# Kernel optimization log

Measured on AMD Instinct MI355X. Metric: run time of the kernel, lower is better.

## Reference

```python
import jax, jax.numpy as jnp
import numpy as np
from jax import lax

FILTER_SIZE = 11
N_ITER = 5


def gaussian_kernel1d(inv_theta, spacing, size):
    # distances = spacing * [-(size//2) .. size//2]; zero out center tap
    d = spacing * jnp.arange(-(size // 2), size // 2 + 1, dtype=jnp.float32)
    k = jnp.exp(-(d * inv_theta) ** 2 / 2)
    return k.at[size // 2].set(0.0)


def conv_along_axis(x, kernel, axis):
    # x: (C, *spatial); 1D conv along `axis`, 'same' padding (kernel symmetric -> corr == conv)
    x = jnp.moveaxis(x, axis, -1)
    shp = x.shape
    x2 = x.reshape(-1, 1, shp[-1])  # (M, 1, L)
    K = kernel.shape[0]
    out = lax.conv_general_dilated(
        x2, kernel[None, None, :].astype(x2.dtype), (1,), [(K // 2, K // 2)],
        dimension_numbers=('NCH', 'OIH', 'NCH'))
    return jnp.moveaxis(out.reshape(shp), -1, axis)


def _gaussian_filter_single(xi, inv_theta, spacing):
    # xi: (C, H, W); separable gaussian with per-sample spacing
    for i in range(2):
        k = gaussian_kernel1d(inv_theta[i], spacing[i], FILTER_SIZE)
        xi = conv_along_axis(xi, k, i + 1)
    return xi


_smooth = jax.vmap(_gaussian_filter_single, in_axes=(0, None, 0))


def reference(x, spatial_spacings, smoothness_weight, inv_smoothness_theta):
    n_classes = x.shape[1]
    comp = -jnp.eye(n_classes, dtype=x.dtype)  # -(label_i == label_j)
    negative_unary = x
    for _ in range(N_ITER):
        p = jax.nn.softmax(x, axis=1)
        s = smoothness_weight * _smooth(p, inv_smoothness_theta, spatial_spacings)
        c = jnp.einsum('bchw,cd->bdhw', s, comp)
        x = negative_unary - c
    return jax.nn.log_softmax(x, axis=1)


def setup_inputs() -> dict:
    key = jax.random.key(0)
    k1, = jax.random.split(key, 1)
    B, C, H, W = 16, 16, 384, 384
    return {
        'x': jax.random.normal(k1, (B, C, H, W), dtype=jnp.float32),
        'spatial_spacings': jnp.ones((B, 2), dtype=jnp.float32),
        'smoothness_weight': jnp.asarray(1.0, dtype=jnp.float32),
        'inv_smoothness_theta': jnp.ones((2,), dtype=jnp.float32),
    }
```

## Files before the change

kernel.cpp:

```cpp
#include <hip/hip_runtime.h>

#define BB 16
#define CC 16
#define HH 384
#define WW 384
#define HWSZ (HH*WW)
#define CHW (CC*HWSZ)
#define NPIX (BB*CHW)

#define FT 768
#define ROWS 12
#define HSEGS (HH/ROWS)
#define SROW 408

typedef unsigned short ushortT;

__device__ __forceinline__ float bf2f(ushortT h) {
    union { unsigned u; float f; } c; c.u = ((unsigned)h) << 16; return c.f;
}
__device__ __forceinline__ ushortT f2bf(float f) {
    union { float f; unsigned u; } c; c.f = f;
    unsigned r = c.u + 0x7FFFu + ((c.u >> 16) & 1u);
    return (ushortT)(r >> 16);
}
__device__ __forceinline__ void unpk2(unsigned u, float& lo, float& hi) {
    union { unsigned u; float f; } a, b;
    a.u = u << 16; b.u = u & 0xFFFF0000u;
    lo = a.f; hi = b.f;
}
__device__ __forceinline__ unsigned pk2(float lo, float hi) {
    return ((unsigned)f2bf(hi) << 16) | (unsigned)f2bf(lo);
}
__device__ __forceinline__ void unpk8(const uint4& q, float* v) {
    unpk2(q.x, v[0], v[1]); unpk2(q.y, v[2], v[3]);
    unpk2(q.z, v[4], v[5]); unpk2(q.w, v[6], v[7]);
}
__device__ __forceinline__ uint4 pk8(const float* v) {
    uint4 q;
    q.x = pk2(v[0], v[1]); q.y = pk2(v[2], v[3]);
    q.z = pk2(v[4], v[5]); q.w = pk2(v[6], v[7]);
    return q;
}

template<int MODE>
__global__ __launch_bounds__(FT) void k_fused(
    const void* __restrict__ in0, const ushortT* __restrict__ x0b,
    void* __restrict__ outp, ushortT* __restrict__ x0b_out,
    const float* __restrict__ spacings, const float* __restrict__ invtheta,
    const float* __restrict__ swp)
{
    __shared__ ushortT xp[2][CC][SROW];
    __shared__ __align__(16) float l_lds[WW];

    const int t  = threadIdx.x;
    const int b  = blockIdx.y;
    const int h0 = blockIdx.x * ROWS;

    if (t < 2 * CC * 12) {
        const int buf = t / (CC * 12);
        const int rem = t - buf * (CC * 12);
        const int c = rem / 12, s = rem - (rem / 12) * 12;
        const int e = (s < 4) ? (2 * s) : (392 + 2 * (s - 4));
        *(unsigned*)&xp[buf][c][e] = 0u;
    }

    const float sw  = swp[0];
    const float sch = spacings[b * 2 + 0] * invtheta[0];
    const float scw = spacings[b * 2 + 1] * invtheta[1];
    float kh[5], kw[5];
#pragma unroll
    for (int j = 0; j < 5; ++j) {
        float dh = sch * (float)(j - 5); kh[j] = __expf(-0.5f * dh * dh);
        float dw = scw * (float)(j - 5); kw[j] = __expf(-0.5f * dw * dw);
    }

    const int ca = t / 48, ga = t - (t / 48) * 48;
    const int colB = t >> 1, halfB = (t & 1) * 8;

    const size_t cbase = (size_t)b * CHW + (size_t)ca * HWSZ + (size_t)ga * 8;

    const uint4 z4 = make_uint4(0u, 0u, 0u, 0u);
    uint4 win[11];
    if (MODE >= 1) {
        const ushortT* tin = (const ushortT*)in0;
#pragma unroll
        for (int j = 0; j < 11; ++j) {
            const int r = h0 + j - 5;
            win[j] = ((unsigned)r < HH) ? *(const uint4*)(tin + cbase + (size_t)r * WW) : z4;
        }
    }

    __syncthreads();

    auto row_body = [&](const int h, const int buf) {
        if (MODE == 0) {
            const float* xf = (const float*)in0;
            const float4 A  = *(const float4*)(xf + cbase + (size_t)h * WW);
            const float4 Bq = *(const float4*)(xf + cbase + (size_t)h * WW + 4);
            float v[8] = {A.x, A.y, A.z, A.w, Bq.x, Bq.y, Bq.z, Bq.w};
            const uint4 q = pk8(v);
            *(uint4*)(x0b_out + cbase + (size_t)h * WW) = q;
            *(uint4*)&xp[buf][ca][8 + ga * 8] = q;
        } else {
            const ushortT* tin = (const ushortT*)in0;
            const int nr = h + 6;
            const uint4 nt = (nr < HH) ? *(const uint4*)(tin + cbase + (size_t)nr * WW) : z4;
            const uint4 uq = *(const uint4*)(x0b + cbase + (size_t)h * WW);
            float acc[8];
#pragma unroll
            for (int k = 0; k < 8; ++k) acc[k] = 0.f;
#pragma unroll
            for (int j = 0; j < 5; ++j) {
                float e1[8], e2[8];
                unpk8(win[j], e1); unpk8(win[10 - j], e2);
                const float kj = kh[j];
#pragma unroll
                for (int k = 0; k < 8; ++k) acc[k] = fmaf(kj, e1[k] + e2[k], acc[k]);
            }
            float uu[8]; unpk8(uq, uu);
            float xv[8];
#pragma unroll
            for (int k = 0; k < 8; ++k) xv[k] = fmaf(sw, acc[k], uu[k]);
            *(uint4*)&xp[buf][ca][8 + ga * 8] = pk8(xv);
#pragma unroll
            for (int j = 0; j < 10; ++j) win[j] = win[j + 1];
            win[10] = nt;
        }
        __syncthreads();

        {
            float xr[8];
#pragma unroll
            for (int cc = 0; cc < 8; ++cc) xr[cc] = bf2f(xp[buf][halfB + cc][8 + colB]);
            float mh = xr[0];
#pragma unroll
            for (int cc = 1; cc < 8; ++cc) mh = fmaxf(mh, xr[cc]);
            const float m = fmaxf(mh, __shfl_xor(mh, 1));
            float e[8]; float shs = 0.f;
#pragma unroll
            for (int cc = 0; cc < 8; ++cc) { e[cc] = __expf(xr[cc] - m); shs += e[cc]; }
            const float s = shs + __shfl_xor(shs, 1);
            if (MODE <= 1) {
                const float inv = 1.0f / s;
#pragma unroll
                for (int cc = 0; cc < 8; ++cc)
                    xp[buf][halfB + cc][8 + colB] = f2bf(e[cc] * inv);
            } else {
                if (!(t & 1)) l_lds[colB] = m + __logf(s);
            }
        }
        __syncthreads();

        if (MODE <= 1) {
            const uint4 q0 = *(const uint4*)&xp[buf][ca][ga * 8];
            const uint4 q1 = *(const uint4*)&xp[buf][ca][ga * 8 + 8];
            const uint4 q2 = *(const uint4*)&xp[buf][ca][ga * 8 + 16];
            float w[24];
            unpk8(q0, w); unpk8(q1, w + 8); unpk8(q2, w + 16);
            float o[8];
#pragma unroll
            for (int k = 0; k < 8; ++k) {
                float a = 0.f;
#pragma unroll
                for (int j = 0; j < 5; ++j)
                    a = fmaf(kw[j], w[k + j + 3] + w[k + 13 - j], a);
                o[k] = a;
            }
            *(uint4*)((ushortT*)outp + cbase + (size_t)h * WW) = pk8(o);
        } else {
            const uint4 xq = *(const uint4*)&xp[buf][ca][8 + ga * 8];
            float xv[8]; unpk8(xq, xv);
            const float4 l0 = *(const float4*)&l_lds[ga * 8];
            const float4 l1 = *(const float4*)&l_lds[ga * 8 + 4];
            float* op = (float*)outp + cbase + (size_t)h * WW;
            *(float4*)op       = make_float4(xv[0]-l0.x, xv[1]-l0.y, xv[2]-l0.z, xv[3]-l0.w);
            *(float4*)(op + 4) = make_float4(xv[4]-l1.x, xv[5]-l1.y, xv[6]-l1.z, xv[7]-l1.w);
        }
    };

    for (int hh = h0; hh < h0 + ROWS; hh += 2) {
        row_body(hh,     0);
        row_body(hh + 1, 1);
    }
}

extern "C" void kernel_launch(void* const* d_in, const int* in_sizes, int n_in,
                              void* d_out, int out_size, void* d_ws, size_t ws_size,
                              hipStream_t stream)
{
    const float* x0   = (const float*)d_in[0];
    const float* spac = (const float*)d_in[1];
    const float* sw   = (const float*)d_in[2];
    const float* it   = (const float*)d_in[3];

    ushortT* tA  = (ushortT*)d_ws;
    ushortT* tB  = tA + (size_t)NPIX;
    ushortT* x0b = tB + (size_t)NPIX;
    float*   out = (float*)d_out;

    dim3 gf(HSEGS, BB);
    dim3 bf(FT);

    k_fused<0><<<gf, bf, 0, stream>>>(x0, nullptr, tA, x0b, spac, it, sw);
    k_fused<1><<<gf, bf, 0, stream>>>(tA, x0b, tB, nullptr, spac, it, sw);
    k_fused<1><<<gf, bf, 0, stream>>>(tB, x0b, tA, nullptr, spac, it, sw);
    k_fused<1><<<gf, bf, 0, stream>>>(tA, x0b, tB, nullptr, spac, it, sw);
    k_fused<1><<<gf, bf, 0, stream>>>(tB, x0b, tA, nullptr, spac, it, sw);
    k_fused<2><<<gf, bf, 0, stream>>>(tA, x0b, out, nullptr, spac, it, sw);
}
```

Measured before the change: 428.9 us.

## Software-pipeline row phases to halve barriers, use DPP reductions and hw bf16 pack

Restructures the per-row loop into a two-row pipelined schedule with quadruple LDS buffers. Stage C of the previous row pair runs alongside stage A of the current pair, so each pair needs only two barriers instead of four per row. The softmax over channels now uses four lanes per column pair with DPP swizzles in place of shfl_xor. Float-to-bf16 packing uses the HIP intrinsic. The trade-off is more LDS use and register pressure from the 12-row window.

```diff
diff --git a/kernel.cpp b/kernel.cpp
--- a/kernel.cpp
+++ b/kernel.cpp
@@ -1,4 +1,5 @@
 #include <hip/hip_runtime.h>
+#include <hip/hip_bf16.h>
 
 #define BB 16
 #define CC 16
@@ -15,21 +16,15 @@
 
 typedef unsigned short ushortT;
 
-__device__ __forceinline__ float bf2f(ushortT h) {
-    union { unsigned u; float f; } c; c.u = ((unsigned)h) << 16; return c.f;
-}
-__device__ __forceinline__ ushortT f2bf(float f) {
-    union { float f; unsigned u; } c; c.f = f;
-    unsigned r = c.u + 0x7FFFu + ((c.u >> 16) & 1u);
-    return (ushortT)(r >> 16);
-}
 __device__ __forceinline__ void unpk2(unsigned u, float& lo, float& hi) {
     union { unsigned u; float f; } a, b;
     a.u = u << 16; b.u = u & 0xFFFF0000u;
     lo = a.f; hi = b.f;
 }
 __device__ __forceinline__ unsigned pk2(float lo, float hi) {
-    return ((unsigned)f2bf(hi) << 16) | (unsigned)f2bf(lo);
+    __hip_bfloat162 h = __float22bfloat162_rn(make_float2(lo, hi));
+    union { __hip_bfloat162 h; unsigned u; } c; c.h = h;
+    return c.u;
 }
 __device__ __forceinline__ void unpk8(const uint4& q, float* v) {
     unpk2(q.x, v[0], v[1]); unpk2(q.y, v[2], v[3]);
@@ -40,6 +35,13 @@
     q.x = pk2(v[0], v[1]); q.y = pk2(v[2], v[3]);
     q.z = pk2(v[4], v[5]); q.w = pk2(v[6], v[7]);
     return q;
+}
+template<int CTRL>
+__device__ __forceinline__ float dpp_f(float x) {
+    union { float f; int i; } c; c.f = x;
+    union { int i; float f; } r;
+    r.i = __builtin_amdgcn_update_dpp(0, c.i, CTRL, 0xF, 0xF, true);
+    return r.f;
 }
 
 template<int MODE>
@@ -49,14 +51,14 @@
     const float* __restrict__ spacings, const float* __restrict__ invtheta,
     const float* __restrict__ swp)
 {
-    __shared__ ushortT xp[2][CC][SROW];
-    __shared__ __align__(16) float l_lds[WW];
+    __shared__ ushortT xp[4][CC][SROW];
+    __shared__ __align__(16) float l_lds[2][WW];
 
     const int t  = threadIdx.x;
     const int b  = blockIdx.y;
     const int h0 = blockIdx.x * ROWS;
 
-    if (t < 2 * CC * 12) {
+    {
         const int buf = t / (CC * 12);
         const int rem = t - buf * (CC * 12);
         const int c = rem / 12, s = rem - (rem / 12) * 12;
@@ -75,82 +77,85 @@
     }
 
     const int ca = t / 48, ga = t - (t / 48) * 48;
-    const int colB = t >> 1, halfB = (t & 1) * 8;
+    const int cp = t >> 2, qq = t & 3;
 
     const size_t cbase = (size_t)b * CHW + (size_t)ca * HWSZ + (size_t)ga * 8;
-
     const uint4 z4 = make_uint4(0u, 0u, 0u, 0u);
-    uint4 win[11];
+
+    uint4 W[12];
     if (MODE >= 1) {
         const ushortT* tin = (const ushortT*)in0;
 #pragma unroll
-        for (int j = 0; j < 11; ++j) {
+        for (int j = 0; j < 12; ++j) {
             const int r = h0 + j - 5;
-            win[j] = ((unsigned)r < HH) ? *(const uint4*)(tin + cbase + (size_t)r * WW) : z4;
+            W[j] = ((unsigned)r < HH) ? *(const uint4*)(tin + cbase + (size_t)r * WW) : z4;
         }
     }
 
     __syncthreads();
 
-    auto row_body = [&](const int h, const int buf) {
-        if (MODE == 0) {
-            const float* xf = (const float*)in0;
-            const float4 A  = *(const float4*)(xf + cbase + (size_t)h * WW);
-            const float4 Bq = *(const float4*)(xf + cbase + (size_t)h * WW + 4);
-            float v[8] = {A.x, A.y, A.z, A.w, Bq.x, Bq.y, Bq.z, Bq.w};
-            const uint4 q = pk8(v);
-            *(uint4*)(x0b_out + cbase + (size_t)h * WW) = q;
-            *(uint4*)&xp[buf][ca][8 + ga * 8] = q;
+    auto A_row_m0 = [&](int h, int buf) {
+        const float* xf = (const float*)in0;
+        const float4 A0 = *(const float4*)(xf + cbase + (size_t)h * WW);
+        const float4 A1 = *(const float4*)(xf + cbase + (size_t)h * WW + 4);
+        float v[8] = {A0.x, A0.y, A0.z, A0.w, A1.x, A1.y, A1.z, A1.w};
+        const uint4 q = pk8(v);
+        *(uint4*)(x0b_out + cbase + (size_t)h * WW) = q;
+        *(uint4*)&xp[buf][ca][8 + ga * 8] = q;
+    };
+
+    auto A_row = [&](int o, int buf, uint4 uq) {
+        float acc[8];
+#pragma unroll
+        for (int k = 0; k < 8; ++k) acc[k] = 0.f;
+#pragma unroll
+        for (int j = 0; j < 5; ++j) {
+            float e1[8], e2[8];
+            unpk8(W[o + j], e1); unpk8(W[o + 10 - j], e2);
+            const float kj = kh[j];
+#pragma unroll
+            for (int k = 0; k < 8; ++k) acc[k] = fmaf(kj, e1[k] + e2[k], acc[k]);
+        }
+        float uu[8]; unpk8(uq, uu);
+        float xv[8];
+#pragma unroll
+        for (int k = 0; k < 8; ++k) xv[k] = fmaf(sw, acc[k], uu[k]);
+        *(uint4*)&xp[buf][ca][8 + ga * 8] = pk8(xv);
+    };
+
+    auto B_row = [&](int buf, int r) {
+        float xa[4], xb[4];
+#pragma unroll
+        for (int i = 0; i < 4; ++i) {
+            const unsigned u = *(const unsigned*)&xp[buf][qq * 4 + i][8 + 2 * cp];
+            unpk2(u, xa[i], xb[i]);
+        }
+        float m0 = fmaxf(fmaxf(xa[0], xa[1]), fmaxf(xa[2], xa[3]));
+        float m1 = fmaxf(fmaxf(xb[0], xb[1]), fmaxf(xb[2], xb[3]));
+        m0 = fmaxf(m0, dpp_f<0xB1>(m0)); m0 = fmaxf(m0, dpp_f<0x4E>(m0));
+        m1 = fmaxf(m1, dpp_f<0xB1>(m1)); m1 = fmaxf(m1, dpp_f<0x4E>(m1));
+        float e0[4], e1[4], s0 = 0.f, s1 = 0.f;
+#pragma unroll
+        for (int i = 0; i < 4; ++i) {
+            e0[i] = __expf(xa[i] - m0); s0 += e0[i];
+            e1[i] = __expf(xb[i] - m1); s1 += e1[i];
+        }
+        s0 += dpp_f<0xB1>(s0); s0 += dpp_f<0x4E>(s0);
+        s1 += dpp_f<0xB1>(s1); s1 += dpp_f<0x4E>(s1);
+        if (MODE <= 1) {
+            const float i0 = 1.0f / s0, i1 = 1.0f / s1;
+#pragma unroll
+            for (int i = 0; i < 4; ++i)
+                *(unsigned*)&xp[buf][qq * 4 + i][8 + 2 * cp] = pk2(e0[i] * i0, e1[i] * i1);
         } else {
-            const ushortT* tin = (const ushortT*)in0;
-            const int nr = h + 6;
-            const uint4 nt = (nr < HH) ? *(const uint4*)(tin + cbase + (size_t)nr * WW) : z4;
-            const uint4 uq = *(const uint4*)(x0b + cbase + (size_t)h * WW);
-            float acc[8];
-#pragma unroll
-            for (int k = 0; k < 8; ++k) acc[k] = 0.f;
-#pragma unroll
-            for (int j = 0; j < 5; ++j) {
-                float e1[8], e2[8];
-                unpk8(win[j], e1); unpk8(win[10 - j], e2);
-                const float kj = kh[j];
-#pragma unroll
-                for (int k = 0; k < 8; ++k) acc[k] = fmaf(kj, e1[k] + e2[k], acc[k]);
-            }
-            float uu[8]; unpk8(uq, uu);
-            float xv[8];
-#pragma unroll
-            for (int k = 0; k < 8; ++k) xv[k] = fmaf(sw, acc[k], uu[k]);
-            *(uint4*)&xp[buf][ca][8 + ga * 8] = pk8(xv);
-#pragma unroll
-            for (int j = 0; j < 10; ++j) win[j] = win[j + 1];
-            win[10] = nt;
-        }
-        __syncthreads();
-
-        {
-            float xr[8];
-#pragma unroll
-            for (int cc = 0; cc < 8; ++cc) xr[cc] = bf2f(xp[buf][halfB + cc][8 + colB]);
-            float mh = xr[0];
-#pragma unroll
-            for (int cc = 1; cc < 8; ++cc) mh = fmaxf(mh, xr[cc]);
-            const float m = fmaxf(mh, __shfl_xor(mh, 1));
-            float e[8]; float shs = 0.f;
-#pragma unroll
-            for (int cc = 0; cc < 8; ++cc) { e[cc] = __expf(xr[cc] - m); shs += e[cc]; }
-            const float s = shs + __shfl_xor(shs, 1);
-            if (MODE <= 1) {
-                const float inv = 1.0f / s;
-#pragma unroll
-                for (int cc = 0; cc < 8; ++cc)
-                    xp[buf][halfB + cc][8 + colB] = f2bf(e[cc] * inv);
-            } else {
-                if (!(t & 1)) l_lds[colB] = m + __logf(s);
-            }
-        }
-        __syncthreads();
-
+            if (qq == 0) {
+                l_lds[r][2 * cp]     = m0 + __logf(s0);
+                l_lds[r][2 * cp + 1] = m1 + __logf(s1);
+            }
+        }
+    };
+
+    auto C_row = [&](int h, int buf, int r) {
         if (MODE <= 1) {
             const uint4 q0 = *(const uint4*)&xp[buf][ca][ga * 8];
             const uint4 q1 = *(const uint4*)&xp[buf][ca][ga * 8 + 8];
@@ -163,25 +168,57 @@
                 float a = 0.f;
 #pragma unroll
                 for (int j = 0; j < 5; ++j)
-                    a = fmaf(kw[j], w[k + j + 3] + w[k + 13 - j], a);
+                    a = fmaf(kw[j], w[k + 3 + j] + w[k + 13 - j], a);
                 o[k] = a;
             }
             *(uint4*)((ushortT*)outp + cbase + (size_t)h * WW) = pk8(o);
         } else {
             const uint4 xq = *(const uint4*)&xp[buf][ca][8 + ga * 8];
             float xv[8]; unpk8(xq, xv);
-            const float4 l0 = *(const float4*)&l_lds[ga * 8];
-            const float4 l1 = *(const float4*)&l_lds[ga * 8 + 4];
+            const float4 l0 = *(const float4*)&l_lds[r][ga * 8];
+            const float4 l1 = *(const float4*)&l_lds[r][ga * 8 + 4];
             float* op = (float*)outp + cbase + (size_t)h * WW;
             *(float4*)op       = make_float4(xv[0]-l0.x, xv[1]-l0.y, xv[2]-l0.z, xv[3]-l0.w);
             *(float4*)(op + 4) = make_float4(xv[4]-l1.x, xv[5]-l1.y, xv[6]-l1.z, xv[7]-l1.w);
         }
     };
 
-    for (int hh = h0; hh < h0 + ROWS; hh += 2) {
-        row_body(hh,     0);
-        row_body(hh + 1, 1);
-    }
+#pragma unroll
+    for (int p = 0; p < 6; ++p) {
+        const int h  = h0 + 2 * p;
+        const int bA = 2 * (p & 1);
+        const int bC = 2 * ((p & 1) ^ 1);
+
+        if (MODE == 0) {
+            if (p > 0) { C_row(h - 2, bC, 0); C_row(h - 1, bC + 1, 1); }
+            A_row_m0(h, bA); A_row_m0(h + 1, bA + 1);
+        } else {
+            if (p > 0) { C_row(h - 2, bC, 0); C_row(h - 1, bC + 1, 1); }
+            const ushortT* tin = (const ushortT*)in0;
+            const uint4 uq0 = *(const uint4*)(x0b + cbase + (size_t)h * WW);
+            const uint4 uq1 = *(const uint4*)(x0b + cbase + (size_t)(h + 1) * WW);
+            uint4 nt0 = z4, nt1 = z4;
+            if (p < 5) {
+                const int r0 = h + 7, r1 = h + 8;
+                if (r0 < HH) nt0 = *(const uint4*)(tin + cbase + (size_t)r0 * WW);
+                if (r1 < HH) nt1 = *(const uint4*)(tin + cbase + (size_t)r1 * WW);
+            }
+            A_row(0, bA,     uq0);
+            A_row(1, bA + 1, uq1);
+            if (p < 5) {
+#pragma unroll
+                for (int j = 0; j < 10; ++j) W[j] = W[j + 2];
+                W[10] = nt0; W[11] = nt1;
+            }
+        }
+        __syncthreads();
+
+        B_row(bA, 0);
+        B_row(bA + 1, 1);
+        __syncthreads();
+    }
+    C_row(h0 + 10, 2, 0);
+    C_row(h0 + 11, 3, 1);
 }
 
 extern "C" void kernel_launch(void* const* d_in, const int* in_sizes, int n_in,
```

Measured after the change: 408.1 us. 1.05x faster.
